# Performance work log

Measured on AMD Instinct MI355X. Metric: run time of the kernel, lower is better.

## Reference

```python
import jax, jax.numpy as jnp
import numpy as np

HEADS = 8
DIM_HEAD = 64
SCALE = DIM_HEAD ** -0.5
POS_DIM = 64


def _sincos_pe(H, W, dim, dtype):
    # matches build_2d_sincos_pos_embed: [1, dim, H, W]
    y = jnp.linspace(-1.0, 1.0, H)[:, None] * jnp.ones((1, W), jnp.float32)
    x = jnp.ones((H, 1), jnp.float32) * jnp.linspace(-1.0, 1.0, W)[None, :]
    omega = 1.0 / (10000.0 ** (jnp.arange(dim // 4, dtype=jnp.float32) / (dim // 4)))
    px = x[..., None] * omega  # [H, W, dim//4]
    py = y[..., None] * omega
    pe = jnp.concatenate([jnp.sin(px), jnp.cos(px), jnp.sin(py), jnp.cos(py)], axis=-1)
    return pe.transpose(2, 0, 1)[None].astype(dtype)


def _conv2d(x, w):
    return jax.lax.conv_general_dilated(
        x, w, (1, 1), 'SAME', dimension_numbers=('NCHW', 'OIHW', 'NCHW'))


def _sobel(d):
    kx = jnp.array([[1, 0, -1], [2, 0, -2], [1, 0, -1]], jnp.float32).reshape(1, 1, 3, 3)
    ky = jnp.array([[1, 2, 1], [0, 0, 0], [-1, -2, -1]], jnp.float32).reshape(1, 1, 3, 3)
    return _conv2d(d, kx), _conv2d(d, ky)


def setup_inputs() -> dict:
    key = jax.random.key(0)
    ks = jax.random.split(key, 8)
    B, C, H, W = 2, 256, 64, 64
    hid = HEADS * DIM_HEAD  # 512
    s = 0.02
    return {
        'x': jax.random.normal(ks[0], (B, C, H, W), jnp.float32),
        'dsm': jax.random.uniform(ks[1], (B, 1, H, W), jnp.float32),
        'wq': jax.random.normal(ks[2], (hid, C), jnp.float32) * s,
        'wkv': jax.random.normal(ks[3], (2 * hid, C + 1), jnp.float32) * s,
        'wout': jax.random.normal(ks[4], (C, hid), jnp.float32) * s,
        'bout': jnp.zeros((C,), jnp.float32),
        'w_hape': jax.random.normal(ks[5], (hid, POS_DIM + 3), jnp.float32) * s,
        'b_hape': jnp.zeros((hid,), jnp.float32),
        'w_alpha': jax.random.normal(ks[6], (1, 1, 3, 3), jnp.float32) * 0.1,
        'b_alpha': jnp.zeros((1,), jnp.float32),
    }


def reference(x, dsm, wq, wkv, wout, bout, w_hape, b_hape, w_alpha, b_alpha):
    B, C, H, W = x.shape
    hid = wq.shape[0]
    # per-sample min-max normalize DSM over spatial dims
    dmin = dsm.min(axis=(2, 3), keepdims=True)
    dmax = dsm.max(axis=(2, 3), keepdims=True)
    d = (dsm - dmin) / (dmax - dmin + 1e-6)
    # HAPE: [PE | h | grad_h] -> 1x1 conv to hidden
    pe = jnp.broadcast_to(_sincos_pe(H, W, POS_DIM, x.dtype), (B, POS_DIM, H, W))
    gx, gy = _sobel(d)
    hape_in = jnp.concatenate([pe, d, gx, gy], axis=1)  # [B, 67, H, W]
    hape_k = jnp.einsum('oc,bchw->bohw', w_hape, hape_in) + b_hape[None, :, None, None]
    # QKV via 1x1 convs
    q = jnp.einsum('oc,bchw->bohw', wq, x)
    kv = jnp.einsum('oc,bchw->bohw', wkv, jnp.concatenate([x, d], axis=1))
    k = kv[:, :hid] + hape_k
    v = kv[:, hid:]
    to_heads = lambda t: t.reshape(B, HEADS, DIM_HEAD, H * W)  # b (h c) x y -> b h c (xy)
    qh = to_heads(q) * SCALE
    kh = to_heads(k)
    vh = to_heads(v)
    sim = jnp.einsum('bhdi,bhdj->bhij', qh, kh)  # [B, h, N, N]
    attn = jax.nn.softmax(sim, axis=-1)
    out = jnp.einsum('bhij,bhdj->bhid', attn, vh)  # [B, h, N, d]
    # b h (x y) d -> b (h d) x y
    out = out.transpose(0, 1, 3, 2).reshape(B, HEADS * DIM_HEAD, H, W)
    out = jnp.einsum('oc,bchw->bohw', wout, out) + bout[None, :, None, None]
    # fine: gradient-magnitude alpha gating
    mag = jnp.sqrt(jnp.maximum(gx, 0.0) ** 2 + jnp.maximum(gy, 0.0) ** 2 + 1e-12)
    alpha = jax.nn.sigmoid(_conv2d(mag, w_alpha) + b_alpha[None, :, None, None])
    return x + out * alpha
```

## Files before the change

### kernel.cpp

```cpp
#include <hip/hip_runtime.h>
#include <math.h>

#define NPOS 4096
#define MTOT 8192
#define KP   352
#define HT 64
#define WT 64

typedef unsigned short ushortT;
typedef short v8s __attribute__((ext_vector_type(8)));
typedef float v4f __attribute__((ext_vector_type(4)));

static __device__ __forceinline__ ushortT bfr(float f) {
    union { float f; unsigned u; } v; v.f = f;
    return (ushortT)((v.u + 0x8000u) >> 16);
}
static __device__ __forceinline__ unsigned pack2bf(float a, float b) {
    union { float f; unsigned u; } ua, ub; ua.f = a; ub.f = b;
    return __builtin_amdgcn_perm(ub.u + 0x8000u, ua.u + 0x8000u, 0x07060302u);
}
static __device__ __forceinline__ float fexp2(float x) {
#if __has_builtin(__builtin_amdgcn_exp2f)
    return __builtin_amdgcn_exp2f(x);
#else
    return exp2f(x);
#endif
}

__global__ void k_minmax(const float* __restrict__ dsm, float* __restrict__ mm) {
    int b = blockIdx.x;
    const float* p = dsm + (size_t)b * NPOS;
    float mn = 1e30f, mx = -1e30f;
    for (int i = threadIdx.x; i < NPOS; i += 256) {
        float v = p[i];
        mn = fminf(mn, v); mx = fmaxf(mx, v);
    }
    for (int off = 32; off; off >>= 1) {
        mn = fminf(mn, __shfl_xor(mn, off, 64));
        mx = fmaxf(mx, __shfl_xor(mx, off, 64));
    }
    __shared__ float smn[4], smx[4];
    int wid = threadIdx.x >> 6;
    if ((threadIdx.x & 63) == 0) { smn[wid] = mn; smx[wid] = mx; }
    __syncthreads();
    if (threadIdx.x == 0) {
        mn = fminf(fminf(smn[0], smn[1]), fminf(smn[2], smn[3]));
        mx = fmaxf(fmaxf(smx[0], smx[1]), fmaxf(smx[2], smx[3]));
        mm[b * 2 + 0] = mn; mm[b * 2 + 1] = mx;
    }
}

__global__ void k_prep(const float* __restrict__ dsm, const float* __restrict__ mm,
                       const float* __restrict__ walpha, const float* __restrict__ balpha,
                       ushortT* __restrict__ F, float* __restrict__ alpha) {
    int idx = blockIdx.x * 256 + threadIdx.x;
    int b = idx / NPOS, n = idx % NPOS;
    int hh = n / WT, ww = n % WT;
    float dmin = mm[b * 2], dmax = mm[b * 2 + 1];
    float inv = 1.0f / (dmax - dmin + 1e-6f);
    const float* dp = dsm + (size_t)b * NPOS;

    float dwin[5][5];
    #pragma unroll
    for (int dy = 0; dy < 5; dy++)
        #pragma unroll
        for (int dx = 0; dx < 5; dx++) {
            int y = hh + dy - 2, x = ww + dx - 2;
            float v = 0.0f;
            if (y >= 0 && y < HT && x >= 0 && x < WT) v = (dp[y * WT + x] - dmin) * inv;
            dwin[dy][dx] = v;
        }

    float gxc = 0.f, gyc = 0.f;
    float conv = 0.f;
    #pragma unroll
    for (int oy = 0; oy < 3; oy++)
        #pragma unroll
        for (int ox = 0; ox < 3; ox++) {
            int qy = hh + oy - 1, qx = ww + ox - 1;
            float m = 0.0f;
            if (qy >= 0 && qy < HT && qx >= 0 && qx < WT) {
                float gx = dwin[oy][ox] - dwin[oy][ox + 2]
                         + 2.f * dwin[oy + 1][ox] - 2.f * dwin[oy + 1][ox + 2]
                         + dwin[oy + 2][ox] - dwin[oy + 2][ox + 2];
                float gy = dwin[oy][ox] + 2.f * dwin[oy][ox + 1] + dwin[oy][ox + 2]
                         - dwin[oy + 2][ox] - 2.f * dwin[oy + 2][ox + 1] - dwin[oy + 2][ox + 2];
                if (oy == 1 && ox == 1) { gxc = gx; gyc = gy; }
                float rx = fmaxf(gx, 0.f), ry = fmaxf(gy, 0.f);
                m = sqrtf(rx * rx + ry * ry + 1e-12f);
            }
            conv += walpha[oy * 3 + ox] * m;
        }
    alpha[idx] = 1.f / (1.f + __expf(-(conv + balpha[0])));

    ushortT* fb = F + (size_t)idx * KP;
    fb[256] = bfr(dwin[2][2]);
    fb[257] = bfr(gxc);
    fb[258] = bfr(gyc);
    float xc = -1.f + 2.f * (float)ww / 63.f;
    float yc = -1.f + 2.f * (float)hh / 63.f;
    #pragma unroll
    for (int i = 0; i < 16; i++) {
        float omega = powf(10000.f, -(float)i / 16.f);
        float px = xc * omega, py = yc * omega;
        fb[259 + i]      = bfr(sinf(px));
        fb[259 + 16 + i] = bfr(cosf(px));
        fb[259 + 32 + i] = bfr(sinf(py));
        fb[259 + 48 + i] = bfr(cosf(py));
    }
    #pragma unroll
    for (int z = 323; z < KP; z++) fb[z] = 0;
}

__global__ void k_cast(const float* __restrict__ x, ushortT* __restrict__ F) {
    __shared__ __align__(16) ushortT Tl[64][72];
    int nt = blockIdx.x * 64;
    int b = blockIdx.y >> 2, ct = (blockIdx.y & 3) * 64;
    int t = threadIdx.x;
    #pragma unroll
    for (int rep = 0; rep < 4; rep++) {
        int row = rep * 16 + (t >> 4), c4 = (t & 15) * 4;
        float4 f4 = *(const float4*)&x[((size_t)(b * 256 + ct + row)) * NPOS + nt + c4];
        Tl[c4 + 0][row] = bfr(f4.x);
        Tl[c4 + 1][row] = bfr(f4.y);
        Tl[c4 + 2][row] = bfr(f4.z);
        Tl[c4 + 3][row] = bfr(f4.w);
    }
    __syncthreads();
    #pragma unroll
    for (int rep = 0; rep < 2; rep++) {
        int slot = rep * 256 + t, row = slot >> 3, c8 = slot & 7;
        *(uint4*)&F[((size_t)(b * 4096 + nt + row)) * KP + ct + c8 * 8] = *(uint4*)&Tl[row][c8 * 8];
    }
}

__global__ void k_wcprep(const float* __restrict__ wq, const float* __restrict__ wkv,
                         const float* __restrict__ whape, const float* __restrict__ bhape,
                         ushortT* __restrict__ Wc, float* __restrict__ biasc) {
    int idx = blockIdx.x * 256 + threadIdx.x;
    int o = idx / KP, k = idx % KP;
    float v = 0.f;
    if (o < 512) {
        if (k < 256) v = wq[o * 256 + k] * 0.18033688011112042f;
        if (k == 0) biasc[o] = 0.f;
    } else if (o < 1024) {
        int r = o - 512;
        if (k < 257) v = wkv[r * 257 + k];
        if (k == 256)      v += whape[r * 67 + 64];
        else if (k == 257) v = whape[r * 67 + 65];
        else if (k == 258) v = whape[r * 67 + 66];
        else if (k >= 259 && k < 323) v = whape[r * 67 + (k - 259)];
        if (k == 0) biasc[o] = bhape[r];
    } else {
        int r = o - 512;
        if (k < 257) v = wkv[r * 257 + k];
        if (k == 0) biasc[o] = 0.f;
    }
    Wc[idx] = bfr(v);
}

__global__ void k_wout(const float* __restrict__ wout, ushortT* __restrict__ woutb) {
    int idx = blockIdx.x * 256 + threadIdx.x;
    woutb[idx] = bfr(wout[idx]);
}

__global__ __launch_bounds__(256) void k_gemm1(const ushortT* __restrict__ Wc, const ushortT* __restrict__ F,
                                               const float* __restrict__ biasc,
                                               ushortT* __restrict__ qT, ushortT* __restrict__ kT,
                                               ushortT* __restrict__ vv) {
    __shared__ __align__(16) ushortT Al[64][40];
    __shared__ __align__(16) ushortT Bl[64][40];
    __shared__ __align__(16) ushortT Vt[64][72];
    int mt = blockIdx.x * 64;
    int ot = blockIdx.y * 64;
    int t = threadIdx.x, w = t >> 6, lane = t & 63, u = lane & 15, quad = lane >> 4;
    int arow = t >> 2, ac8 = t & 3;
    v4f acc[4] = {};
    for (int k0 = 0; k0 < KP; k0 += 32) {
        __syncthreads();
        *(uint4*)&Al[arow][ac8 * 8] = *(const uint4*)&Wc[(size_t)(ot + arow) * KP + k0 + ac8 * 8];
        *(uint4*)&Bl[arow][ac8 * 8] = *(const uint4*)&F[(size_t)(mt + arow) * KP + k0 + ac8 * 8];
        __syncthreads();
        v8s a = *(v8s*)&Al[w * 16 + u][quad * 8];
        #pragma unroll
        for (int n4 = 0; n4 < 4; n4++) {
            v8s bb = *(v8s*)&Bl[n4 * 16 + u][quad * 8];
            acc[n4] = __builtin_amdgcn_mfma_f32_16x16x32_bf16(a, bb, acc[n4], 0, 0, 0);
        }
    }
    int obase = ot + w * 16 + quad * 4;
    float bo[4];
    #pragma unroll
    for (int r = 0; r < 4; r++) bo[r] = biasc[obase + r];
    if (ot < 1024) {
        int h = (ot >> 6) & 7;
        ushortT* dst = (ot < 512) ? qT : kT;
        #pragma unroll
        for (int n4 = 0; n4 < 4; n4++) {
            int m = mt + n4 * 16 + u;
            uint2 val;
            val.x = pack2bf(acc[n4][0] + bo[0], acc[n4][1] + bo[1]);
            val.y = pack2bf(acc[n4][2] + bo[2], acc[n4][3] + bo[3]);
            *(uint2*)&dst[((size_t)h * MTOT + m) * 64 + w * 16 + quad * 4] = val;
        }
    } else {
        __syncthreads();
        #pragma unroll
        for (int n4 = 0; n4 < 4; n4++) {
            int ml = n4 * 16 + u;
            #pragma unroll
            for (int r = 0; r < 4; r++) Vt[w * 16 + quad * 4 + r][ml] = bfr(acc[n4][r] + bo[r]);
        }
        __syncthreads();
        #pragma unroll
        for (int rep = 0; rep < 2; rep++) {
            int slot = rep * 256 + t, row = slot >> 3, c8 = slot & 7;
            *(uint4*)&vv[(size_t)(ot - 1024 + row) * MTOT + mt + c8 * 8] = *(uint4*)&Vt[row][c8 * 8];
        }
    }
}

#define LIDX(row, cb) (((row) << 6) + ((((cb) ^ ((row) & 7))) << 3))
__global__ __launch_bounds__(256, 4) void k_flash(const ushortT* __restrict__ qT,
                                                  const ushortT* __restrict__ kT,
                                                  const ushortT* __restrict__ vv,
                                                  ushortT* __restrict__ aoB) {
    __shared__ __align__(16) ushortT QP[128 * 64];
    __shared__ __align__(16) ushortT Kl[64 * 64];
    __shared__ __align__(16) ushortT Vl[64 * 64];

    int it = blockIdx.x;
    int bh = blockIdx.y;
    int b = bh >> 3, h = bh & 7;
    int colbase = b * NPOS;
    int t = threadIdx.x, w = t >> 6, lane = t & 63, u = lane & 15, quad = lane >> 4;
    const ushortT* Qg = qT + ((size_t)h * MTOT + colbase + it * 128) * 64;
    const ushortT* Kg = kT + ((size_t)h * MTOT + colbase) * 64;
    const ushortT* Vg = vv + (size_t)(h * 64) * MTOT + colbase;

    #pragma unroll
    for (int z = 0; z < 4; z++) {
        int slot = z * 256 + t, row = slot >> 3, cb = slot & 7;
        *(uint4*)&QP[LIDX(row, cb)] = *(const uint4*)&Qg[(size_t)row * 64 + cb * 8];
    }
    __syncthreads();
    v8s bq[2][2];
    #pragma unroll
    for (int g = 0; g < 2; g++)
        #pragma unroll
        for (int hf = 0; hf < 2; hf++)
            bq[g][hf] = *(v8s*)&QP[LIDX(w * 32 + g * 16 + u, hf * 4 + quad)];

    float li[2] = {0.f, 0.f};
    v4f O[4][2] = {};

    for (int jc = 0; jc < 64; jc++) {
        int jb = jc * 64;
        __syncthreads();
        #pragma unroll
        for (int z = 0; z < 2; z++) {
            int slot = z * 256 + t, row = slot >> 3, cb = slot & 7;
            *(uint4*)&Kl[LIDX(row, cb)] = *(const uint4*)&Kg[(size_t)(jb + row) * 64 + cb * 8];
            *(uint4*)&Vl[LIDX(row, cb)] = *(const uint4*)&Vg[(size_t)row * MTOT + jb + cb * 8];
        }
        __syncthreads();

        v4f st[4][2] = {};
        #pragma unroll
        for (int k4 = 0; k4 < 4; k4++) {
            v8s ak0 = *(v8s*)&Kl[LIDX(k4 * 16 + u, quad)];
            v8s ak1 = *(v8s*)&Kl[LIDX(k4 * 16 + u, 4 + quad)];
            #pragma unroll
            for (int g = 0; g < 2; g++) {
                st[k4][g] = __builtin_amdgcn_mfma_f32_16x16x32_bf16(ak0, bq[g][0], st[k4][g], 0, 0, 0);
                st[k4][g] = __builtin_amdgcn_mfma_f32_16x16x32_bf16(ak1, bq[g][1], st[k4][g], 0, 0, 0);
            }
        }

        #pragma unroll
        for (int g = 0; g < 2; g++) {
            int prow = w * 32 + g * 16 + u;
            #pragma unroll
            for (int k4 = 0; k4 < 4; k4++) {
                float p0 = fexp2(st[k4][g][0]);
                float p1 = fexp2(st[k4][g][1]);
                float p2 = fexp2(st[k4][g][2]);
                float p3 = fexp2(st[k4][g][3]);
                li[g] += (p0 + p1) + (p2 + p3);
                uint2 pv; pv.x = pack2bf(p0, p1); pv.y = pack2bf(p2, p3);
                *(uint2*)&QP[LIDX(prow, k4 * 2 + (quad >> 1)) + (quad & 1) * 4] = pv;
            }
        }
        v8s bp[2][2];
        #pragma unroll
        for (int g = 0; g < 2; g++)
            #pragma unroll
            for (int ks = 0; ks < 2; ks++)
                bp[g][ks] = *(v8s*)&QP[LIDX(w * 32 + g * 16 + u, ks * 4 + quad)];
        #pragma unroll
        for (int d4 = 0; d4 < 4; d4++) {
            v8s av0 = *(v8s*)&Vl[LIDX(d4 * 16 + u, quad)];
            v8s av1 = *(v8s*)&Vl[LIDX(d4 * 16 + u, 4 + quad)];
            #pragma unroll
            for (int g = 0; g < 2; g++) {
                O[d4][g] = __builtin_amdgcn_mfma_f32_16x16x32_bf16(av0, bp[g][0], O[d4][g], 0, 0, 0);
                O[d4][g] = __builtin_amdgcn_mfma_f32_16x16x32_bf16(av1, bp[g][1], O[d4][g], 0, 0, 0);
            }
        }
    }

    #pragma unroll
    for (int g = 0; g < 2; g++) {
        li[g] += __shfl_xor(li[g], 16, 64);
        li[g] += __shfl_xor(li[g], 32, 64);
        float inv = 1.f / li[g];
        size_t base = (size_t)(colbase + it * 128 + w * 32 + g * 16 + u) * 512 + h * 64;
        #pragma unroll
        for (int d4 = 0; d4 < 4; d4++) {
            uint2 val;
            val.x = pack2bf(O[d4][g][0] * inv, O[d4][g][1] * inv);
            val.y = pack2bf(O[d4][g][2] * inv, O[d4][g][3] * inv);
            *(uint2*)&aoB[base + d4 * 16 + quad * 4] = val;
        }
    }
}

__global__ __launch_bounds__(256) void k_gemm2(const ushortT* __restrict__ woutb, const ushortT* __restrict__ aoB,
                                               const float* __restrict__ bout, const float* __restrict__ x,
                                               const float* __restrict__ alpha, float* __restrict__ out) {
    __shared__ __align__(16) ushortT Al[64][40];
    __shared__ __align__(16) ushortT Bl[64][40];
    int mt = blockIdx.x * 64;
    int ot = blockIdx.y * 64;
    int t = threadIdx.x, w = t >> 6, lane = t & 63, u = lane & 15, quad = lane >> 4;
    int arow = t >> 2, ac8 = t & 3;
    v4f acc[4] = {};
    for (int k0 = 0; k0 < 512; k0 += 32) {
        __syncthreads();
        *(uint4*)&Al[arow][ac8 * 8] = *(const uint4*)&woutb[(size_t)(ot + arow) * 512 + k0 + ac8 * 8];
        *(uint4*)&Bl[arow][ac8 * 8] = *(const uint4*)&aoB[(size_t)(mt + arow) * 512 + k0 + ac8 * 8];
        __syncthreads();
        v8s a = *(v8s*)&Al[w * 16 + u][quad * 8];
        #pragma unroll
        for (int n4 = 0; n4 < 4; n4++) {
            v8s bb = *(v8s*)&Bl[n4 * 16 + u][quad * 8];
            acc[n4] = __builtin_amdgcn_mfma_f32_16x16x32_bf16(a, bb, acc[n4], 0, 0, 0);
        }
    }
    int b = mt >> 12, n0 = mt & 4095;
    int obase = ot + w * 16 + quad * 4;
    float bo[4];
    #pragma unroll
    for (int r = 0; r < 4; r++) bo[r] = bout[obase + r];
    #pragma unroll
    for (int n4 = 0; n4 < 4; n4++) {
        int n = n0 + n4 * 16 + u;
        float al = alpha[(size_t)b * NPOS + n];
        #pragma unroll
        for (int r = 0; r < 4; r++) {
            size_t xi = ((size_t)(b * 256 + obase + r)) * NPOS + n;
            out[xi] = x[xi] + (acc[n4][r] + bo[r]) * al;
        }
    }
}

extern "C" void kernel_launch(void* const* d_in, const int* in_sizes, int n_in,
                              void* d_out, int out_size, void* d_ws, size_t ws_size,
                              hipStream_t stream) {
    const float* x      = (const float*)d_in[0];
    const float* dsm    = (const float*)d_in[1];
    const float* wq     = (const float*)d_in[2];
    const float* wkv    = (const float*)d_in[3];
    const float* wout   = (const float*)d_in[4];
    const float* bout   = (const float*)d_in[5];
    const float* whape  = (const float*)d_in[6];
    const float* bhape  = (const float*)d_in[7];
    const float* walpha = (const float*)d_in[8];
    const float* balpha = (const float*)d_in[9];
    float* out = (float*)d_out;
    float* ws  = (float*)d_ws;

    size_t off = 0;
    float* mm    = ws + off; off += 256;
    float* alpha = ws + off; off += (size_t)2 * NPOS;
    float* biasc = ws + off; off += 2048;
    ushortT* F     = (ushortT*)(ws + off); off += (size_t)MTOT * KP / 2;
    ushortT* Wc    = (ushortT*)(ws + off); off += (size_t)1536 * KP / 2;
    ushortT* woutb = (ushortT*)(ws + off); off += (size_t)256 * 512 / 2;
    ushortT* qT    = (ushortT*)(ws + off); off += (size_t)8 * MTOT * 64 / 2;
    ushortT* kT    = (ushortT*)(ws + off); off += (size_t)8 * MTOT * 64 / 2;
    ushortT* vv    = (ushortT*)(ws + off); off += (size_t)512 * MTOT / 2;
    ushortT* aoB   = (ushortT*)(ws + off); off += (size_t)MTOT * 512 / 2;
    (void)in_sizes; (void)n_in; (void)out_size; (void)ws_size;

    k_minmax<<<2, 256, 0, stream>>>(dsm, mm);
    k_prep<<<32, 256, 0, stream>>>(dsm, mm, walpha, balpha, F, alpha);
    k_cast<<<dim3(64, 8), 256, 0, stream>>>(x, F);
    k_wcprep<<<(1536 * KP) / 256, 256, 0, stream>>>(wq, wkv, whape, bhape, Wc, biasc);
    k_wout<<<512, 256, 0, stream>>>(wout, woutb);
    k_gemm1<<<dim3(128, 24), 256, 0, stream>>>(Wc, F, biasc, qT, kT, vv);
    k_flash<<<dim3(32, 16), 256, 0, stream>>>(qT, kT, vv, aoB);
    k_gemm2<<<dim3(128, 4), 256, 0, stream>>>(woutb, aoB, bout, x, alpha, out);
}
```

Before: 235.2 us.

## Restructure flash kernel to per-wave 64-query tiles with direct global K/V loads

The attention kernel now gives each wave 64 query rows (256 per block) and loads K and V fragments straight from global memory into registers, dropping the shared K/V staging and both block barriers per key chunk. P stays in a per-wave LDS buffer, bf16 packing of P switches to truncation, and the grid halves to 256 blocks with launch bounds lowered to 2. The prep kernel also swaps powf/sinf/cosf for exp2f and fast intrinsics. This removes barrier stalls, but each wave re-reads K/V through cache with no block sharing, and register pressure and halved occupancy increase.

Result: slower. 273.8 us (+16.4%).

```diff
diff --git a/kernel.cpp b/kernel.cpp
--- a/kernel.cpp
+++ b/kernel.cpp
@@ -18,6 +18,10 @@
 static __device__ __forceinline__ unsigned pack2bf(float a, float b) {
     union { float f; unsigned u; } ua, ub; ua.f = a; ub.f = b;
     return __builtin_amdgcn_perm(ub.u + 0x8000u, ua.u + 0x8000u, 0x07060302u);
+}
+static __device__ __forceinline__ unsigned pack2bf_t(float a, float b) {
+    union { float f; unsigned u; } ua, ub; ua.f = a; ub.f = b;
+    return __builtin_amdgcn_perm(ub.u, ua.u, 0x07060302u);
 }
 static __device__ __forceinline__ float fexp2(float x) {
 #if __has_builtin(__builtin_amdgcn_exp2f)
@@ -99,14 +103,15 @@
     fb[258] = bfr(gyc);
     float xc = -1.f + 2.f * (float)ww / 63.f;
     float yc = -1.f + 2.f * (float)hh / 63.f;
+    const float l2w = 13.287712379549449f;
     #pragma unroll
     for (int i = 0; i < 16; i++) {
-        float omega = powf(10000.f, -(float)i / 16.f);
+        float omega = exp2f(-(float)i * (l2w / 16.f));
         float px = xc * omega, py = yc * omega;
-        fb[259 + i]      = bfr(sinf(px));
-        fb[259 + 16 + i] = bfr(cosf(px));
-        fb[259 + 32 + i] = bfr(sinf(py));
-        fb[259 + 48 + i] = bfr(cosf(py));
+        fb[259 + i]      = bfr(__sinf(px));
+        fb[259 + 16 + i] = bfr(__cosf(px));
+        fb[259 + 32 + i] = bfr(__sinf(py));
+        fb[259 + 48 + i] = bfr(__cosf(py));
     }
     #pragma unroll
     for (int z = 323; z < KP; z++) fb[z] = 0;
@@ -221,100 +226,90 @@
 }
 
 #define LIDX(row, cb) (((row) << 6) + ((((cb) ^ ((row) & 7))) << 3))
-__global__ __launch_bounds__(256, 4) void k_flash(const ushortT* __restrict__ qT,
+__global__ __launch_bounds__(256, 2) void k_flash(const ushortT* __restrict__ qT,
                                                   const ushortT* __restrict__ kT,
                                                   const ushortT* __restrict__ vv,
                                                   ushortT* __restrict__ aoB) {
-    __shared__ __align__(16) ushortT QP[128 * 64];
-    __shared__ __align__(16) ushortT Kl[64 * 64];
-    __shared__ __align__(16) ushortT Vl[64 * 64];
+    __shared__ __align__(16) ushortT Pw[4][64 * 64];
 
     int it = blockIdx.x;
     int bh = blockIdx.y;
     int b = bh >> 3, h = bh & 7;
     int colbase = b * NPOS;
     int t = threadIdx.x, w = t >> 6, lane = t & 63, u = lane & 15, quad = lane >> 4;
-    const ushortT* Qg = qT + ((size_t)h * MTOT + colbase + it * 128) * 64;
+    int qb = it * 256 + w * 64;
+
+    const ushortT* Qg = qT + ((size_t)h * MTOT + colbase + qb) * 64;
     const ushortT* Kg = kT + ((size_t)h * MTOT + colbase) * 64;
-    const ushortT* Vg = vv + (size_t)(h * 64) * MTOT + colbase;
-
-    #pragma unroll
-    for (int z = 0; z < 4; z++) {
-        int slot = z * 256 + t, row = slot >> 3, cb = slot & 7;
-        *(uint4*)&QP[LIDX(row, cb)] = *(const uint4*)&Qg[(size_t)row * 64 + cb * 8];
-    }
-    __syncthreads();
-    v8s bq[2][2];
-    #pragma unroll
-    for (int g = 0; g < 2; g++)
+    const ushortT* Vg = vv + ((size_t)(h * 64)) * MTOT + colbase;
+    ushortT* P = &Pw[w][0];
+
+    v8s bq[4][2];
+    #pragma unroll
+    for (int g = 0; g < 4; g++)
         #pragma unroll
         for (int hf = 0; hf < 2; hf++)
-            bq[g][hf] = *(v8s*)&QP[LIDX(w * 32 + g * 16 + u, hf * 4 + quad)];
-
-    float li[2] = {0.f, 0.f};
-    v4f O[4][2] = {};
+            bq[g][hf] = *(const v8s*)&Qg[(size_t)(g * 16 + u) * 64 + hf * 32 + quad * 8];
+
+    float li[4] = {0.f, 0.f, 0.f, 0.f};
+    v4f O[4][4] = {};
 
     for (int jc = 0; jc < 64; jc++) {
         int jb = jc * 64;
-        __syncthreads();
-        #pragma unroll
-        for (int z = 0; z < 2; z++) {
-            int slot = z * 256 + t, row = slot >> 3, cb = slot & 7;
-            *(uint4*)&Kl[LIDX(row, cb)] = *(const uint4*)&Kg[(size_t)(jb + row) * 64 + cb * 8];
-            *(uint4*)&Vl[LIDX(row, cb)] = *(const uint4*)&Vg[(size_t)row * MTOT + jb + cb * 8];
-        }
-        __syncthreads();
-
-        v4f st[4][2] = {};
+        v8s ka[4][2], va[4][2];
+        #pragma unroll
+        for (int k4 = 0; k4 < 4; k4++)
+            #pragma unroll
+            for (int hf = 0; hf < 2; hf++)
+                ka[k4][hf] = *(const v8s*)&Kg[(size_t)(jb + k4 * 16 + u) * 64 + hf * 32 + quad * 8];
+        #pragma unroll
+        for (int d4 = 0; d4 < 4; d4++)
+            #pragma unroll
+            for (int ks = 0; ks < 2; ks++)
+                va[d4][ks] = *(const v8s*)&Vg[(size_t)(d4 * 16 + u) * MTOT + jb + ks * 32 + quad * 8];
+
         #pragma unroll
         for (int k4 = 0; k4 < 4; k4++) {
-            v8s ak0 = *(v8s*)&Kl[LIDX(k4 * 16 + u, quad)];
-            v8s ak1 = *(v8s*)&Kl[LIDX(k4 * 16 + u, 4 + quad)];
-            #pragma unroll
-            for (int g = 0; g < 2; g++) {
-                st[k4][g] = __builtin_amdgcn_mfma_f32_16x16x32_bf16(ak0, bq[g][0], st[k4][g], 0, 0, 0);
-                st[k4][g] = __builtin_amdgcn_mfma_f32_16x16x32_bf16(ak1, bq[g][1], st[k4][g], 0, 0, 0);
+            v4f st[4];
+            #pragma unroll
+            for (int g = 0; g < 4; g++) {
+                st[g] = (v4f){0.f, 0.f, 0.f, 0.f};
+                st[g] = __builtin_amdgcn_mfma_f32_16x16x32_bf16(ka[k4][0], bq[g][0], st[g], 0, 0, 0);
+                st[g] = __builtin_amdgcn_mfma_f32_16x16x32_bf16(ka[k4][1], bq[g][1], st[g], 0, 0, 0);
             }
-        }
-
-        #pragma unroll
-        for (int g = 0; g < 2; g++) {
-            int prow = w * 32 + g * 16 + u;
-            #pragma unroll
-            for (int k4 = 0; k4 < 4; k4++) {
-                float p0 = fexp2(st[k4][g][0]);
-                float p1 = fexp2(st[k4][g][1]);
-                float p2 = fexp2(st[k4][g][2]);
-                float p3 = fexp2(st[k4][g][3]);
+            #pragma unroll
+            for (int g = 0; g < 4; g++) {
+                float p0 = fexp2(st[g][0]);
+                float p1 = fexp2(st[g][1]);
+                float p2 = fexp2(st[g][2]);
+                float p3 = fexp2(st[g][3]);
                 li[g] += (p0 + p1) + (p2 + p3);
-                uint2 pv; pv.x = pack2bf(p0, p1); pv.y = pack2bf(p2, p3);
-                *(uint2*)&QP[LIDX(prow, k4 * 2 + (quad >> 1)) + (quad & 1) * 4] = pv;
+                uint2 pv; pv.x = pack2bf_t(p0, p1); pv.y = pack2bf_t(p2, p3);
+                *(uint2*)&P[LIDX(g * 16 + u, k4 * 2 + (quad >> 1)) + (quad & 1) * 4] = pv;
             }
         }
-        v8s bp[2][2];
-        #pragma unroll
-        for (int g = 0; g < 2; g++)
+
+        v8s bp[4][2];
+        #pragma unroll
+        for (int g = 0; g < 4; g++)
             #pragma unroll
             for (int ks = 0; ks < 2; ks++)
-                bp[g][ks] = *(v8s*)&QP[LIDX(w * 32 + g * 16 + u, ks * 4 + quad)];
-        #pragma unroll
-        for (int d4 = 0; d4 < 4; d4++) {
-            v8s av0 = *(v8s*)&Vl[LIDX(d4 * 16 + u, quad)];
-            v8s av1 = *(v8s*)&Vl[LIDX(d4 * 16 + u, 4 + quad)];
-            #pragma unroll
-            for (int g = 0; g < 2; g++) {
-                O[d4][g] = __builtin_amdgcn_mfma_f32_16x16x32_bf16(av0, bp[g][0], O[d4][g], 0, 0, 0);
-                O[d4][g] = __builtin_amdgcn_mfma_f32_16x16x32_bf16(av1, bp[g][1], O[d4][g], 0, 0, 0);
+                bp[g][ks] = *(v8s*)&P[LIDX(g * 16 + u, ks * 4 + quad)];
+        #pragma unroll
+        for (int d4 = 0; d4 < 4; d4++)
+            #pragma unroll
+            for (int g = 0; g < 4; g++) {
+                O[d4][g] = __builtin_amdgcn_mfma_f32_16x16x32_bf16(va[d4][0], bp[g][0], O[d4][g], 0, 0, 0);
+                O[d4][g] = __builtin_amdgcn_mfma_f32_16x16x32_bf16(va[d4][1], bp[g][1], O[d4][g], 0, 0, 0);
             }
-        }
-    }
-
-    #pragma unroll
-    for (int g = 0; g < 2; g++) {
+    }
+
+    #pragma unroll
+    for (int g = 0; g < 4; g++) {
         li[g] += __shfl_xor(li[g], 16, 64);
         li[g] += __shfl_xor(li[g], 32, 64);
         float inv = 1.f / li[g];
-        size_t base = (size_t)(colbase + it * 128 + w * 32 + g * 16 + u) * 512 + h * 64;
+        size_t base = (size_t)(colbase + qb + g * 16 + u) * 512 + h * 64;
         #pragma unroll
         for (int d4 = 0; d4 < 4; d4++) {
             uint2 val;
@@ -399,6 +394,6 @@
     k_wcprep<<<(1536 * KP) / 256, 256, 0, stream>>>(wq, wkv, whape, bhape, Wc, biasc);
     k_wout<<<512, 256, 0, stream>>>(wout, woutb);
     k_gemm1<<<dim3(128, 24), 256, 0, stream>>>(Wc, F, biasc, qT, kT, vv);
-    k_flash<<<dim3(32, 16), 256, 0, stream>>>(qT, kT, vv, aoB);
+    k_flash<<<dim3(16, 16), 256, 0, stream>>>(qT, kT, vv, aoB);
     k_gemm2<<<dim3(128, 4), 256, 0, stream>>>(woutb, aoB, bout, x, alpha, out);
 }
```
